# Optimization experiments

Measured on AMD Instinct MI355X. Metric: run time of the kernel, lower is better.

The kernel has to match this reference:

```python
import jax, jax.numpy as jnp
import numpy as np

B, IN_C, H, W = 64, 64, 32, 32
OUT_C, KH, KW = 64, 3, 3
STRIDE, PAD, DIL = 1, 1, 1
OUT_H = (H + 2 * PAD - DIL * (KH - 1) - 1) // STRIDE + 1  # 32
OUT_W = (W + 2 * PAD - DIL * (KW - 1) - 1) // STRIDE + 1  # 32


def setup_inputs() -> dict:
    key = jax.random.key(0)
    kx, kw, kb = jax.random.split(key, 3)
    x = jax.random.normal(kx, (B, IN_C, H, W), dtype=jnp.float32)
    n = IN_C * KH * KW
    stdv = 1.0 / np.sqrt(n)
    weight = jax.random.uniform(kw, (OUT_H, OUT_W, OUT_C, IN_C, KH, KW),
                                dtype=jnp.float32, minval=-stdv, maxval=stdv)
    bias = jax.random.uniform(kb, (OUT_C, OUT_H, OUT_W),
                              dtype=jnp.float32, minval=-stdv, maxval=stdv)
    return {"x": x, "weight": weight, "bias": bias}


def _im2col(x):
    # x: [B, C, H, W] -> cols: [B, C*KH*KW, OUT_H*OUT_W], torch.unfold channel-major order
    xp = jnp.pad(x, ((0, 0), (0, 0), (PAD, PAD), (PAD, PAD)))
    patches = []
    for kh in range(KH):
        for kw in range(KW):
            h0, w0 = kh * DIL, kw * DIL
            patches.append(xp[:, :,
                              h0:h0 + (OUT_H - 1) * STRIDE + 1:STRIDE,
                              w0:w0 + (OUT_W - 1) * STRIDE + 1:STRIDE])
    cols = jnp.stack(patches, axis=2)  # [B, C, KH*KW, OUT_H, OUT_W]
    return cols.reshape(x.shape[0], x.shape[1] * KH * KW, OUT_H * OUT_W)


def reference(x, weight, bias):
    cols = _im2col(x)  # [B, K, L] with K = inC*kH*kW, L = outH*outW
    w = weight.reshape(OUT_H * OUT_W, OUT_C, IN_C * KH * KW)  # [L, outC, K]
    # per-location matmul: out[b, l, o] = sum_k cols[b, k, l] * w[l, o, k]
    out = jnp.einsum('bkl,lok->blo', cols, w)
    out = out.reshape(x.shape[0], OUT_H, OUT_W, OUT_C).transpose(0, 3, 1, 2)
    return out + bias[None]
```

## Files before the change

kernel.cpp:

```cpp
#include <hip/hip_runtime.h>
#include <hip/hip_bf16.h>

typedef __attribute__((ext_vector_type(8))) short short8;
typedef __attribute__((ext_vector_type(4))) float f32x4;

__device__ __forceinline__ unsigned short f2bf(float f) {
    union { float f; unsigned int u; } v; v.f = f;
    unsigned int u = v.u;
    u = (u + 0x7FFFu + ((u >> 16) & 1u)) >> 16;
    return (unsigned short)u;
}

__global__ __launch_bounds__(256) void k_xt(const float* __restrict__ x,
                                            unsigned short* __restrict__ xt) {
    const int h  = blockIdx.x;
    const int cg = blockIdx.y;
    const int t  = threadIdx.x;
    __shared__ unsigned short L[32 * 520];

    #pragma unroll
    for (int i = 0; i < 16; ++i) {
        int s   = t + i * 256;
        int row = s >> 3;
        int wq  = s & 7;
        int b = row >> 3, c = row & 7;
        const f32x4 v = *(const f32x4*)(x + (((size_t)(b * 64 + cg * 8 + c) * 32 + h) * 32 + wq * 4));
        int base = c * 64 + b;
        L[(wq * 4 + 0) * 520 + base] = f2bf(v[0]);
        L[(wq * 4 + 1) * 520 + base] = f2bf(v[1]);
        L[(wq * 4 + 2) * 520 + base] = f2bf(v[2]);
        L[(wq * 4 + 3) * 520 + base] = f2bf(v[3]);
    }
    __syncthreads();
    #pragma unroll
    for (int i = 0; i < 8; ++i) {
        int s  = t + i * 256;
        int w  = s >> 6;
        int ch = s & 63;
        short8 v = *(const short8*)&L[w * 520 + ch * 8];
        *(short8*)(xt + (((size_t)(h * 32 + w) * 64 + cg * 8) * 64 + ch * 8)) = v;
    }
}

__global__ __launch_bounds__(256) void k_main(const float* __restrict__ wgt,
                                              const unsigned short* __restrict__ xt,
                                              const float* __restrict__ bias,
                                              float* __restrict__ ws2) {
    const int l  = blockIdx.x;
    const int oh = l >> 5, ow = l & 31;
    const int t  = threadIdx.x;
    const int wave = t >> 6, lane = t & 63;
    const int wm = wave >> 1, wn = wave & 1;

    __shared__ unsigned short Ash[64 * 72];
    __shared__ unsigned short Bsh[64 * 72];

    f32x4 acc[2][2];
    #pragma unroll
    for (int i = 0; i < 2; ++i)
        #pragma unroll
        for (int j = 0; j < 2; ++j)
            acc[i][j] = (f32x4){0.f, 0.f, 0.f, 0.f};

    const float* wslab = wgt + (size_t)l * (64 * 576);
    const int b0 = wave * 16;
    const int o  = t >> 2, kp = t & 3;

    for (int kt = 0; kt < 9; ++kt) {
        {
            int kk = kt * 64 + lane;
            int c  = kk / 9;
            int r  = kk - c * 9;
            int kh = r / 3;
            int kw = r - kh * 3;
            int hh = oh + kh - 1;
            int ww = ow + kw - 1;
            short8 va = {0,0,0,0,0,0,0,0};
            short8 vb = {0,0,0,0,0,0,0,0};
            if ((unsigned)hh < 32u && (unsigned)ww < 32u) {
                const unsigned short* src = xt + (((size_t)(hh * 32 + ww) * 64 + c) * 64 + b0);
                va = *(const short8*)src;
                vb = *(const short8*)(src + 8);
            }
            #pragma unroll
            for (int j = 0; j < 8; ++j) Ash[(b0 + j) * 72 + lane] = (unsigned short)va[j];
            #pragma unroll
            for (int j = 0; j < 8; ++j) Ash[(b0 + 8 + j) * 72 + lane] = (unsigned short)vb[j];
        }
        {
            const f32x4* bp = (const f32x4*)(wslab + o * 576 + kt * 64 + kp * 16);
            f32x4 f0 = bp[0], f1 = bp[1], f2 = bp[2], f3 = bp[3];
            short8 p0, p1;
            p0[0] = (short)f2bf(f0[0]); p0[1] = (short)f2bf(f0[1]);
            p0[2] = (short)f2bf(f0[2]); p0[3] = (short)f2bf(f0[3]);
            p0[4] = (short)f2bf(f1[0]); p0[5] = (short)f2bf(f1[1]);
            p0[6] = (short)f2bf(f1[2]); p0[7] = (short)f2bf(f1[3]);
            p1[0] = (short)f2bf(f2[0]); p1[1] = (short)f2bf(f2[1]);
            p1[2] = (short)f2bf(f2[2]); p1[3] = (short)f2bf(f2[3]);
            p1[4] = (short)f2bf(f3[0]); p1[5] = (short)f2bf(f3[1]);
            p1[6] = (short)f2bf(f3[2]); p1[7] = (short)f2bf(f3[3]);
            unsigned short* bdst = &Bsh[o * 72 + kp * 16];
            *(short8*)bdst       = p0;
            *(short8*)(bdst + 8) = p1;
        }
        __syncthreads();
        #pragma unroll
        for (int ks = 0; ks < 2; ++ks) {
            int kof = ks * 32 + (lane >> 4) * 8;
            short8 a0 = *(const short8*)&Ash[(wm * 32 + (lane & 15)) * 72 + kof];
            short8 a1 = *(const short8*)&Ash[(wm * 32 + 16 + (lane & 15)) * 72 + kof];
            short8 q0 = *(const short8*)&Bsh[(wn * 32 + (lane & 15)) * 72 + kof];
            short8 q1 = *(const short8*)&Bsh[(wn * 32 + 16 + (lane & 15)) * 72 + kof];
            acc[0][0] = __builtin_amdgcn_mfma_f32_16x16x32_bf16(a0, q0, acc[0][0], 0, 0, 0);
            acc[0][1] = __builtin_amdgcn_mfma_f32_16x16x32_bf16(a0, q1, acc[0][1], 0, 0, 0);
            acc[1][0] = __builtin_amdgcn_mfma_f32_16x16x32_bf16(a1, q0, acc[1][0], 0, 0, 0);
            acc[1][1] = __builtin_amdgcn_mfma_f32_16x16x32_bf16(a1, q1, acc[1][1], 0, 0, 0);
        }
        __syncthreads();
    }

    const int col = lane & 15;
    const int rq  = (lane >> 4) * 4;
    #pragma unroll
    for (int j = 0; j < 2; ++j) {
        int n = wn * 32 + j * 16 + col;
        float bv = bias[n * 1024 + l];
        #pragma unroll
        for (int i = 0; i < 2; ++i) {
            int mbase = wm * 32 + i * 16 + rq;
            #pragma unroll
            for (int q = 0; q < 4; ++q) {
                ws2[(size_t)l * 4096 + (size_t)(mbase + q) * 64 + n] = acc[i][j][q] + bv;
            }
        }
    }
}

__global__ __launch_bounds__(256) void k_out(const float* __restrict__ ws2,
                                             float* __restrict__ out) {
    const int bx = blockIdx.x;
    const int lt = bx & 15;
    const int mt = bx >> 4;
    const int t  = threadIdx.x;
    __shared__ float T[64 * 65];
    const int l0 = lt * 64, m0 = mt * 64;

    #pragma unroll
    for (int i = 0; i < 16; ++i) {
        int lr = (t >> 6) + i * 4;
        int m  = t & 63;
        T[lr * 65 + m] = ws2[(size_t)(l0 + lr) * 4096 + m0 + m];
    }
    __syncthreads();
    #pragma unroll
    for (int i = 0; i < 16; ++i) {
        int mr = (t >> 6) + i * 4;
        int lc = t & 63;
        out[(size_t)(m0 + mr) * 1024 + l0 + lc] = T[lc * 65 + mr];
    }
}

__global__ __launch_bounds__(256) void k_naive(const float* __restrict__ x,
                                               const float* __restrict__ wgt,
                                               const float* __restrict__ bias,
                                               float* __restrict__ out) {
    int idx = blockIdx.x * 256 + threadIdx.x;
    int ow = idx & 31, oh = (idx >> 5) & 31, o = (idx >> 10) & 63, b = idx >> 16;
    float acc = bias[(o * 32 + oh) * 32 + ow];
    const float* wp = wgt + ((size_t)(oh * 32 + ow) * 64 + o) * 576;
    for (int c = 0; c < 64; ++c) {
        for (int kh = 0; kh < 3; ++kh) {
            int hh = oh + kh - 1;
            if ((unsigned)hh >= 32u) continue;
            for (int kw = 0; kw < 3; ++kw) {
                int ww = ow + kw - 1;
                if ((unsigned)ww >= 32u) continue;
                acc += x[((size_t)(b * 64 + c) * 32 + hh) * 32 + ww] * wp[c * 9 + kh * 3 + kw];
            }
        }
    }
    out[idx] = acc;
}

extern "C" void kernel_launch(void* const* d_in, const int* in_sizes, int n_in,
                              void* d_out, int out_size, void* d_ws, size_t ws_size,
                              hipStream_t stream) {
    const float* x    = (const float*)d_in[0];
    const float* wgt  = (const float*)d_in[1];
    const float* bias = (const float*)d_in[2];
    float* out = (float*)d_out;

    const size_t xt_bytes  = (size_t)32 * 32 * 64 * 64 * 2;
    const size_t ws2_bytes = (size_t)1024 * 4096 * 4;

    if (ws_size >= xt_bytes + ws2_bytes) {
        unsigned short* xt = (unsigned short*)d_ws;
        float* ws2 = (float*)((char*)d_ws + xt_bytes);
        k_xt<<<dim3(32, 8), 256, 0, stream>>>(x, xt);
        k_main<<<1024, 256, 0, stream>>>(wgt, xt, bias, ws2);
        k_out<<<1024, 256, 0, stream>>>(ws2, out);
    } else {
        k_naive<<<(64 * 64 * 32 * 32) / 256, 256, 0, stream>>>(x, wgt, bias, out);
    }
}
```

Measured before the change: 48.60 us.

## Double-buffer k_main tiles, remap block order, store intermediate in bf16

The main kernel now prefetches the next K-tile's input and weight data into registers while the current tile is staged into one of two shared-memory buffers. That lets it drop the second barrier per iteration. Blocks are remapped so consecutive block IDs map to spatial locations 128 apart. The intermediate result is written as bf16 instead of fp32, which halves the traffic written by k_main and read by k_out, and k_out now uses vectorized loads and stores. The bf16 intermediate adds another rounding step to the output, and the extra prefetch registers may reduce occupancy.

```diff
diff --git a/kernel.cpp b/kernel.cpp
--- a/kernel.cpp
+++ b/kernel.cpp
@@ -45,15 +45,16 @@
 __global__ __launch_bounds__(256) void k_main(const float* __restrict__ wgt,
                                               const unsigned short* __restrict__ xt,
                                               const float* __restrict__ bias,
-                                              float* __restrict__ ws2) {
-    const int l  = blockIdx.x;
+                                              unsigned short* __restrict__ ws2b) {
+    const int bid = blockIdx.x;
+    const int l   = (bid & 7) * 128 + (bid >> 3);
     const int oh = l >> 5, ow = l & 31;
     const int t  = threadIdx.x;
     const int wave = t >> 6, lane = t & 63;
     const int wm = wave >> 1, wn = wave & 1;
 
-    __shared__ unsigned short Ash[64 * 72];
-    __shared__ unsigned short Bsh[64 * 72];
+    __shared__ unsigned short Ash[2][64 * 72];
+    __shared__ unsigned short Bsh[2][64 * 72];
 
     f32x4 acc[2][2];
     #pragma unroll
@@ -65,58 +66,78 @@
     const float* wslab = wgt + (size_t)l * (64 * 576);
     const int b0 = wave * 16;
     const int o  = t >> 2, kp = t & 3;
+    const float* bbase = wslab + o * 576 + kp * 16;
+
+    auto loadA = [&](int kt, short8& va, short8& vb) {
+        int kk = kt * 64 + lane;
+        int c  = kk / 9;
+        int r  = kk - c * 9;
+        int kh = r / 3;
+        int kw = r - kh * 3;
+        int hh = oh + kh - 1;
+        int ww = ow + kw - 1;
+        va = (short8){0,0,0,0,0,0,0,0};
+        vb = (short8){0,0,0,0,0,0,0,0};
+        if ((unsigned)hh < 32u && (unsigned)ww < 32u) {
+            const unsigned short* src = xt + (((size_t)(hh * 32 + ww) * 64 + c) * 64 + b0);
+            va = *(const short8*)src;
+            vb = *(const short8*)(src + 8);
+        }
+    };
+    auto loadB = [&](int kt, f32x4& w0, f32x4& w1, f32x4& w2, f32x4& w3) {
+        const f32x4* bp = (const f32x4*)(bbase + kt * 64);
+        w0 = bp[0]; w1 = bp[1]; w2 = bp[2]; w3 = bp[3];
+    };
+
+    short8 cA0, cA1;
+    short8 nA0 = (short8){0,0,0,0,0,0,0,0}, nA1 = (short8){0,0,0,0,0,0,0,0};
+    f32x4 cB0, cB1, cB2, cB3;
+    f32x4 nB0 = (f32x4){0,0,0,0}, nB1 = nB0, nB2 = nB0, nB3 = nB0;
+
+    loadA(0, cA0, cA1);
+    loadB(0, cB0, cB1, cB2, cB3);
 
     for (int kt = 0; kt < 9; ++kt) {
+        const int p = kt & 1;
+        if (kt < 8) {
+            loadA(kt + 1, nA0, nA1);
+            loadB(kt + 1, nB0, nB1, nB2, nB3);
+        }
+        #pragma unroll
+        for (int j = 0; j < 8; ++j) Ash[p][(b0 + j) * 72 + lane] = (unsigned short)cA0[j];
+        #pragma unroll
+        for (int j = 0; j < 8; ++j) Ash[p][(b0 + 8 + j) * 72 + lane] = (unsigned short)cA1[j];
         {
-            int kk = kt * 64 + lane;
-            int c  = kk / 9;
-            int r  = kk - c * 9;
-            int kh = r / 3;
-            int kw = r - kh * 3;
-            int hh = oh + kh - 1;
-            int ww = ow + kw - 1;
-            short8 va = {0,0,0,0,0,0,0,0};
-            short8 vb = {0,0,0,0,0,0,0,0};
-            if ((unsigned)hh < 32u && (unsigned)ww < 32u) {
-                const unsigned short* src = xt + (((size_t)(hh * 32 + ww) * 64 + c) * 64 + b0);
-                va = *(const short8*)src;
-                vb = *(const short8*)(src + 8);
-            }
-            #pragma unroll
-            for (int j = 0; j < 8; ++j) Ash[(b0 + j) * 72 + lane] = (unsigned short)va[j];
-            #pragma unroll
-            for (int j = 0; j < 8; ++j) Ash[(b0 + 8 + j) * 72 + lane] = (unsigned short)vb[j];
-        }
-        {
-            const f32x4* bp = (const f32x4*)(wslab + o * 576 + kt * 64 + kp * 16);
-            f32x4 f0 = bp[0], f1 = bp[1], f2 = bp[2], f3 = bp[3];
             short8 p0, p1;
-            p0[0] = (short)f2bf(f0[0]); p0[1] = (short)f2bf(f0[1]);
-            p0[2] = (short)f2bf(f0[2]); p0[3] = (short)f2bf(f0[3]);
-            p0[4] = (short)f2bf(f1[0]); p0[5] = (short)f2bf(f1[1]);
-            p0[6] = (short)f2bf(f1[2]); p0[7] = (short)f2bf(f1[3]);
-            p1[0] = (short)f2bf(f2[0]); p1[1] = (short)f2bf(f2[1]);
-            p1[2] = (short)f2bf(f2[2]); p1[3] = (short)f2bf(f2[3]);
-            p1[4] = (short)f2bf(f3[0]); p1[5] = (short)f2bf(f3[1]);
-            p1[6] = (short)f2bf(f3[2]); p1[7] = (short)f2bf(f3[3]);
-            unsigned short* bdst = &Bsh[o * 72 + kp * 16];
+            p0[0] = (short)f2bf(cB0[0]); p0[1] = (short)f2bf(cB0[1]);
+            p0[2] = (short)f2bf(cB0[2]); p0[3] = (short)f2bf(cB0[3]);
+            p0[4] = (short)f2bf(cB1[0]); p0[5] = (short)f2bf(cB1[1]);
+            p0[6] = (short)f2bf(cB1[2]); p0[7] = (short)f2bf(cB1[3]);
+            p1[0] = (short)f2bf(cB2[0]); p1[1] = (short)f2bf(cB2[1]);
+            p1[2] = (short)f2bf(cB2[2]); p1[3] = (short)f2bf(cB2[3]);
+            p1[4] = (short)f2bf(cB3[0]); p1[5] = (short)f2bf(cB3[1]);
+            p1[6] = (short)f2bf(cB3[2]); p1[7] = (short)f2bf(cB3[3]);
+            unsigned short* bdst = &Bsh[p][o * 72 + kp * 16];
             *(short8*)bdst       = p0;
             *(short8*)(bdst + 8) = p1;
         }
-        __syncthreads();
+        asm volatile("s_waitcnt lgkmcnt(0)" ::: "memory");
+        __builtin_amdgcn_s_barrier();
+        __builtin_amdgcn_sched_barrier(0);
         #pragma unroll
         for (int ks = 0; ks < 2; ++ks) {
             int kof = ks * 32 + (lane >> 4) * 8;
-            short8 a0 = *(const short8*)&Ash[(wm * 32 + (lane & 15)) * 72 + kof];
-            short8 a1 = *(const short8*)&Ash[(wm * 32 + 16 + (lane & 15)) * 72 + kof];
-            short8 q0 = *(const short8*)&Bsh[(wn * 32 + (lane & 15)) * 72 + kof];
-            short8 q1 = *(const short8*)&Bsh[(wn * 32 + 16 + (lane & 15)) * 72 + kof];
+            short8 a0 = *(const short8*)&Ash[p][(wm * 32 + (lane & 15)) * 72 + kof];
+            short8 a1 = *(const short8*)&Ash[p][(wm * 32 + 16 + (lane & 15)) * 72 + kof];
+            short8 q0 = *(const short8*)&Bsh[p][(wn * 32 + (lane & 15)) * 72 + kof];
+            short8 q1 = *(const short8*)&Bsh[p][(wn * 32 + 16 + (lane & 15)) * 72 + kof];
             acc[0][0] = __builtin_amdgcn_mfma_f32_16x16x32_bf16(a0, q0, acc[0][0], 0, 0, 0);
             acc[0][1] = __builtin_amdgcn_mfma_f32_16x16x32_bf16(a0, q1, acc[0][1], 0, 0, 0);
             acc[1][0] = __builtin_amdgcn_mfma_f32_16x16x32_bf16(a1, q0, acc[1][0], 0, 0, 0);
             acc[1][1] = __builtin_amdgcn_mfma_f32_16x16x32_bf16(a1, q1, acc[1][1], 0, 0, 0);
         }
-        __syncthreads();
+        cA0 = nA0; cA1 = nA1;
+        cB0 = nB0; cB1 = nB1; cB2 = nB2; cB3 = nB3;
     }
 
     const int col = lane & 15;
@@ -130,13 +151,13 @@
             int mbase = wm * 32 + i * 16 + rq;
             #pragma unroll
             for (int q = 0; q < 4; ++q) {
-                ws2[(size_t)l * 4096 + (size_t)(mbase + q) * 64 + n] = acc[i][j][q] + bv;
+                ws2b[(size_t)l * 4096 + (size_t)(mbase + q) * 64 + n] = f2bf(acc[i][j][q] + bv);
             }
         }
     }
 }
 
-__global__ __launch_bounds__(256) void k_out(const float* __restrict__ ws2,
+__global__ __launch_bounds__(256) void k_out(const unsigned short* __restrict__ ws2b,
                                              float* __restrict__ out) {
     const int bx = blockIdx.x;
     const int lt = bx & 15;
@@ -146,17 +167,30 @@
     const int l0 = lt * 64, m0 = mt * 64;
 
     #pragma unroll
-    for (int i = 0; i < 16; ++i) {
-        int lr = (t >> 6) + i * 4;
-        int m  = t & 63;
-        T[lr * 65 + m] = ws2[(size_t)(l0 + lr) * 4096 + m0 + m];
+    for (int i = 0; i < 2; ++i) {
+        int s  = t + i * 256;
+        int lr = s >> 3;
+        int mc = (s & 7) * 8;
+        short8 v = *(const short8*)&ws2b[(size_t)(l0 + lr) * 4096 + m0 + mc];
+        #pragma unroll
+        for (int j = 0; j < 8; ++j) {
+            union { unsigned int u; float f; } w;
+            w.u = ((unsigned int)(unsigned short)v[j]) << 16;
+            T[lr * 65 + mc + j] = w.f;
+        }
     }
     __syncthreads();
     #pragma unroll
-    for (int i = 0; i < 16; ++i) {
-        int mr = (t >> 6) + i * 4;
-        int lc = t & 63;
-        out[(size_t)(m0 + mr) * 1024 + l0 + lc] = T[lc * 65 + mr];
+    for (int i = 0; i < 4; ++i) {
+        int s  = t + i * 256;
+        int mr = s >> 4;
+        int lc = (s & 15) * 4;
+        f32x4 v;
+        v[0] = T[(lc + 0) * 65 + mr];
+        v[1] = T[(lc + 1) * 65 + mr];
+        v[2] = T[(lc + 2) * 65 + mr];
+        v[3] = T[(lc + 3) * 65 + mr];
+        *(f32x4*)(out + (size_t)(m0 + mr) * 1024 + l0 + lc) = v;
     }
 }
 
@@ -191,14 +225,14 @@
     float* out = (float*)d_out;
 
     const size_t xt_bytes  = (size_t)32 * 32 * 64 * 64 * 2;
-    const size_t ws2_bytes = (size_t)1024 * 4096 * 4;
+    const size_t ws2_bytes = (size_t)1024 * 4096 * 2;
 
     if (ws_size >= xt_bytes + ws2_bytes) {
-        unsigned short* xt = (unsigned short*)d_ws;
-        float* ws2 = (float*)((char*)d_ws + xt_bytes);
+        unsigned short* xt   = (unsigned short*)d_ws;
+        unsigned short* ws2b = (unsigned short*)((char*)d_ws + xt_bytes);
         k_xt<<<dim3(32, 8), 256, 0, stream>>>(x, xt);
-        k_main<<<1024, 256, 0, stream>>>(wgt, xt, bias, ws2);
-        k_out<<<1024, 256, 0, stream>>>(ws2, out);
+        k_main<<<1024, 256, 0, stream>>>(wgt, xt, bias, ws2b);
+        k_out<<<1024, 256, 0, stream>>>(ws2b, out);
     } else {
         k_naive<<<(64 * 64 * 32 * 32) / 256, 256, 0, stream>>>(x, wgt, bias, out);
     }
```

New measurement: 46.12 us. 5.1% less time.
